# Kernel tuning notes

Measured on AMD Instinct MI355X. Metric: run time of the kernel, lower is better.

Reference implementation:

```python
import jax, jax.numpy as jnp
import numpy as np

EPS = 1e-5
ADJ = 33  # fixed adjusted effective kernel (odd, in [7, 2*ks]); see notes
G, GP = 8, 16  # groups, group_planes


def setup_inputs() -> dict:
    key = jax.random.key(0)
    ks = jax.random.split(key, 6)
    N, C, H, W = 8, 128, 64, 64
    return {
        'x': jax.random.normal(ks[0], (N, C, H, W), jnp.float32),
        'qkv_w': jax.random.normal(ks[1], (2 * C, C), jnp.float32) * (1.0 / np.sqrt(C)),
        'bn_qkv_g': jnp.ones((2 * C,), jnp.float32),
        'bn_qkv_b': jnp.zeros((2 * C,), jnp.float32),
        'base_relative': jax.random.normal(ks[2], (2 * GP, 2 * H - 1, 2 * H - 1), jnp.float32),
        'bn_sim_g': jnp.ones((3 * G,), jnp.float32),
        'bn_sim_b': jnp.zeros((3 * G,), jnp.float32),
        'bn_out_g': jnp.ones((2 * C,), jnp.float32),
        'bn_out_b': jnp.zeros((2 * C,), jnp.float32),
        'in_g': jnp.ones((C,), jnp.float32),
        'in_b': jnp.zeros((C,), jnp.float32),
        'mlp_w1': jax.random.normal(ks[3], (4 * C, C), jnp.float32) * (1.0 / np.sqrt(C)),
        'mlp_w2': jax.random.normal(ks[4], (C, 4 * C), jnp.float32) * (1.0 / np.sqrt(4 * C)),
    }


def _axis_attention(x, qkv_w, bn_qkv_g, bn_qkv_b, base_relative, bn_sim_g, bn_sim_b, bn_out_g, bn_out_b):
    N, C, H, W = x.shape
    out = C
    # height attention: (N,C,H,W) -> (N,W,C,H) -> (N*W, C, H)
    xp = jnp.transpose(x, (0, 3, 1, 2)).reshape(N * W, C, H)
    qkv = jnp.einsum('oc,bcl->bol', qkv_w, xp)
    # BatchNorm1d (training-mode batch stats over (batch, length))
    m = qkv.mean((0, 2), keepdims=True)
    v = qkv.var((0, 2), keepdims=True)
    qkv = (qkv - m) * jax.lax.rsqrt(v + EPS) * bn_qkv_g[None, :, None] + bn_qkv_b[None, :, None]
    qkv = qkv.reshape(N * W, G, 2 * GP, H)
    q, k, vv = qkv[:, :, :GP // 2], qkv[:, :, GP // 2:GP], qkv[:, :, GP:]
    # relative position encodings, bilinear resize (half-pixel == align_corners=False)
    pos = jax.image.resize(base_relative, (2 * GP, ADJ, ADJ), method='bilinear')
    q_e, k_e, v_e = pos[:GP // 2], pos[GP // 2:GP], pos[GP:]
    # resize q/k/v along the attended axis H -> ADJ (1D linear)
    rs = lambda t: jax.image.resize(t, t.shape[:-1] + (ADJ,), method='linear')
    qa, ka, va = rs(q), rs(k), rs(vv)
    qr = jnp.einsum('bgci,cij->bgij', qa, q_e)
    kr = jnp.einsum('bgci,cij->bgij', ka, k_e).transpose(0, 1, 3, 2)
    qk = jnp.einsum('bgci,bgcj->bgij', qa, ka)
    sim = jnp.concatenate([qk, qr, kr], axis=1)  # (N*W, 3G, A, A)
    # BatchNorm2d with per-original-sample stats (torch loop applies BN per b over (W, A, A))
    sim = sim.reshape(N, W, 3 * G, ADJ, ADJ)
    m = sim.mean((1, 3, 4), keepdims=True)
    v2 = sim.var((1, 3, 4), keepdims=True)
    sim = (sim - m) * jax.lax.rsqrt(v2 + EPS) * bn_sim_g[None, None, :, None, None] + bn_sim_b[None, None, :, None, None]
    sim = sim.reshape(N, W, 3, G, ADJ, ADJ).sum(2)  # (N,W,G,A,A)
    # resize similarity maps back to (H,H), then softmax over keys
    sim = jax.image.resize(sim, (N, W, G, H, H), method='bilinear')
    sim = jax.nn.softmax(sim, axis=-1)
    # v embedding resized to (H,H); v resized back to length H
    v_eH = jax.image.resize(v_e, (GP, H, H), method='bilinear')
    vb = jax.image.resize(va, va.shape[:-1] + (H,), method='linear').reshape(N, W, G, GP, H)
    sv = jnp.einsum('nwgij,nwgcj->nwgci', sim, vb)
    sve = jnp.einsum('nwgij,cij->nwgci', sim, v_eH)
    so = jnp.concatenate([sv, sve], axis=-1).reshape(N * W, 2 * out, H)
    m = so.mean((0, 2), keepdims=True)
    v3 = so.var((0, 2), keepdims=True)
    so = (so - m) * jax.lax.rsqrt(v3 + EPS) * bn_out_g[None, :, None] + bn_out_b[None, :, None]
    o = so.reshape(N, W, out, 2, H).sum(3)  # (N,W,out,H)
    return jnp.transpose(o, (0, 2, 3, 1))   # (N,out,H,W)


def _spatial_block(o, in_g, in_b, mlp_w1, mlp_w2):
    N, C, H, W = o.shape
    each = C // 12   # each_direction_channels (deterministic, see notes)
    step = 2         # min(max_dilation=2, min(H,W)//8)
    base = o[:, :each]
    zw = jnp.zeros_like(base[..., :step])
    zh = jnp.zeros_like(base[:, :, :step])
    r = jnp.concatenate([zw, base[..., :-step]], axis=-1)
    l = jnp.concatenate([base[..., step:], zw], axis=-1)
    d = jnp.concatenate([zh, base[:, :, :-step]], axis=2)
    u = jnp.concatenate([base[:, :, step:], zh], axis=2)
    xo = jnp.concatenate([r, l, d, u, o[:, 4 * each:]], axis=1)  # still C channels
    # affine InstanceNorm2d
    m = xo.mean((2, 3), keepdims=True)
    v = xo.var((2, 3), keepdims=True)
    xn = (xo - m) * jax.lax.rsqrt(v + EPS) * in_g[None, :, None, None] + in_b[None, :, None, None]
    h1 = jax.nn.gelu(jnp.einsum('oc,nchw->nohw', mlp_w1, xn), approximate=False)
    return jnp.einsum('oc,nchw->nohw', mlp_w2, h1) + o


def reference(x, qkv_w, bn_qkv_g, bn_qkv_b, base_relative, bn_sim_g, bn_sim_b,
              bn_out_g, bn_out_b, in_g, in_b, mlp_w1, mlp_w2):
    o = _axis_attention(x, qkv_w, bn_qkv_g, bn_qkv_b, base_relative,
                        bn_sim_g, bn_sim_b, bn_out_g, bn_out_b)
    return _spatial_block(o, in_g, in_b, mlp_w1, mlp_w2)
```

## Files before the change

### kernel.cpp

```cpp
#include <hip/hip_runtime.h>
#include <math.h>

constexpr float EPSV = 1e-5f;
typedef unsigned short u16;
using bf16x8 = __attribute__((ext_vector_type(8))) short;
using f32x4  = __attribute__((ext_vector_type(4))) float;

constexpr size_t F_W127  = 0;
constexpr size_t F_W64   = F_W127 + 4224;
constexpr size_t F_QKVST = F_W64  + 2112;
constexpr size_t F_SIMST = F_QKVST+ 512;
constexpr size_t F_SOST  = F_SIMST+ 384;
constexpr size_t F_INST  = F_SOST + 512;
constexpr size_t F_POSTMP= F_INST + 2048;
constexpr size_t F_POS   = F_POSTMP + 134112;
constexpr size_t F_QKV   = F_POS  + 34848;
constexpr size_t F_QKVR  = F_QKV  + 8388608;
constexpr size_t F_SIM   = F_QKVR + 4325376;
constexpr size_t F_PART6 = F_SIM  + 13381632;
constexpr size_t F_VEH   = F_PART6 + 4460544;
constexpr size_t F_XNT   = F_VEH  + 33792;
constexpr size_t F_KET   = F_XNT  + 2097152;
constexpr size_t F_SO    = F_QKV;
constexpr size_t F_XQ    = F_SIM;
constexpr size_t F_BNP2  = F_PART6 + 262144;
constexpr size_t F_WQB   = F_PART6 + 524288;
constexpr size_t F_H1    = F_SIM + 4194304;
constexpr size_t F_W1B   = F_POSTMP;
constexpr size_t F_W2B   = F_POSTMP + 32768;

__device__ __forceinline__ u16 f2b(float x){
  unsigned u = __float_as_uint(x);
  return (u16)((u + 0x7FFFu + ((u>>16)&1u)) >> 16);
}
__device__ __forceinline__ float b2f(u16 v){
  return __uint_as_float((unsigned)v << 16);
}

__device__ __forceinline__ float gelu_f(float v){
  float x = v*0.70710678f;
  float ax = fabsf(x);
  float t = __frcp_rn(1.0f + 0.3275911f*ax);
  float p = 1.061405429f;
  p = p*t - 1.453152027f;
  p = p*t + 1.421413741f;
  p = p*t - 0.284496736f;
  p = p*t + 0.254829592f;
  p = p*t;
  float e = __expf(-ax*ax);
  float y = 1.0f - p*e;
  float er = copysignf(y, x);
  return 0.5f*v*(1.0f + er);
}

struct UpT { int j0[64]; float fj[64]; };
constexpr UpT mkUp(){
  UpT t{};
  for (int o=0;o<64;++o){
    float x = ((float)o + 0.5f)*0.515625f - 0.5f;
    if (x < 0.f) x = 0.f;
    if (x > 32.f) x = 32.f;
    int j = (int)x; if (j > 31) j = 31;
    t.j0[o] = j; t.fj[o] = x - (float)j;
  }
  return t;
}
constexpr UpT UT = mkUp();

__device__ __forceinline__ void upfac(int o, int& j0, float& f){
  float x = ((float)o + 0.5f)*0.515625f - 0.5f;
  x = fminf(fmaxf(x, 0.f), 32.f);
  int j = (int)x; j = j < 31 ? j : 31;
  j0 = j; f = x - (float)j;
}

__device__ __forceinline__ void fma8(float (&a)[8], float qv, const float4& q0, const float4& q1){
  a[0] += qv*q0.x; a[1] += qv*q0.y; a[2] += qv*q0.z; a[3] += qv*q0.w;
  a[4] += qv*q1.x; a[5] += qv*q1.y; a[6] += qv*q1.z; a[7] += qv*q1.w;
}
__device__ __forceinline__ void fma8h(float (&a)[8], float qv, uint4 u){
  a[0] += qv*b2f((u16)(u.x&0xFFFFu)); a[1] += qv*b2f((u16)(u.x>>16));
  a[2] += qv*b2f((u16)(u.y&0xFFFFu)); a[3] += qv*b2f((u16)(u.y>>16));
  a[4] += qv*b2f((u16)(u.z&0xFFFFu)); a[5] += qv*b2f((u16)(u.z>>16));
  a[6] += qv*b2f((u16)(u.w&0xFFFFu)); a[7] += qv*b2f((u16)(u.w>>16));
}

__global__ void k_tables(float* __restrict__ W127, float* __restrict__ W64){
  int i = threadIdx.x;
  if (i < 33){
    const float inv = 127.0f/33.0f;
    float x = ((float)i + 0.5f)*inv - 0.5f;
    float s = 0.f;
    for (int j=0;j<127;++j){ float w = 1.0f - fabsf((float)j - x)/inv; w = fmaxf(w,0.f); W127[i*127+j]=w; s+=w; }
    float r = 1.0f/s;
    for (int j=0;j<127;++j) W127[i*127+j] *= r;
  } else if (i < 66){
    int ii = i-33;
    const float inv = 64.0f/33.0f;
    float x = ((float)ii + 0.5f)*inv - 0.5f;
    float s=0.f;
    for (int j=0;j<64;++j){ float w = 1.0f - fabsf((float)j - x)/inv; w=fmaxf(w,0.f); W64[ii*64+j]=w; s+=w; }
    float r=1.0f/s;
    for (int j=0;j<64;++j) W64[ii*64+j]*=r;
  }
}

__global__ void k_cvtb(const float* __restrict__ src, u16* __restrict__ dst, int n){
  int id = blockIdx.x*256 + threadIdx.x;
  if (id < n) dst[id] = f2b(src[id]);
}

__global__ __launch_bounds__(256) void k_xt(const float* __restrict__ x, u16* __restrict__ xq){
  __shared__ float T[128][66];
  int n = blockIdx.x>>6, h = blockIdx.x&63;
  int tid = threadIdx.x;
  for (int e=tid;e<8192;e+=256){
    int c = e>>6, w = e&63;
    T[c][w] = x[(((size_t)(n*128+c))*64 + h)*64 + w];
  }
  __syncthreads();
  for (int e=tid;e<8192;e+=256){
    int w = e>>7, c = e&127;
    xq[(((size_t)(n*64+w))*64 + h)*128 + c] = f2b(T[c][w]);
  }
}

__global__ __launch_bounds__(256) void k_qkv(const u16* __restrict__ xq, const u16* __restrict__ wqb,
                                             u16* __restrict__ qkvT, float2* __restrict__ part){
  int b = blockIdx.x;
  int tid = threadIdx.x;
  int wv = tid>>6, l = tid&63;
  int wn = wv*64;
  int lr = l&15, lq = l>>4;
  __shared__ u16 As[64*40];
  __shared__ u16 Bs[256*40];
  f32x4 acc[4][4];
  #pragma unroll
  for (int mi=0;mi<4;++mi)
    #pragma unroll
    for (int ni=0;ni<4;++ni) acc[mi][ni] = (f32x4){0.f,0.f,0.f,0.f};
  const u16* Ag = xq + (size_t)b*8192;
  const u16* Bg = wqb;
  for (int ks=0; ks<128; ks+=32){
    __syncthreads();
    { int e = tid; int row = e>>2, q = e&3;
      *(uint4*)&As[row*40 + q*8] = *(const uint4*)&Ag[(size_t)row*128 + ks + q*8]; }
    #pragma unroll
    for (int p=0;p<4;++p){
      int e = tid + p*256; int row = e>>2, q = e&3;
      *(uint4*)&Bs[row*40 + q*8] = *(const uint4*)&Bg[(size_t)row*128 + ks + q*8];
    }
    __syncthreads();
    bf16x8 af[4], bfr[4];
    #pragma unroll
    for (int mi=0;mi<4;++mi) af[mi] = *(const bf16x8*)&As[(mi*16 + lr)*40 + lq*8];
    #pragma unroll
    for (int ni=0;ni<4;++ni) bfr[ni] = *(const bf16x8*)&Bs[(wn + ni*16 + lr)*40 + lq*8];
    #pragma unroll
    for (int mi=0;mi<4;++mi)
      #pragma unroll
      for (int ni=0;ni<4;++ni)
        acc[mi][ni] = __builtin_amdgcn_mfma_f32_16x16x32_bf16(af[mi], bfr[ni], acc[mi][ni], 0,0,0);
  }
  float cs[4] = {0.f,0.f,0.f,0.f}, cq[4] = {0.f,0.f,0.f,0.f};
  u16* ob = qkvT + (size_t)b*16384;
  #pragma unroll
  for (int mi=0;mi<4;++mi)
    #pragma unroll
    for (int r=0;r<4;++r){
      int row = mi*16 + lq*4 + r;
      #pragma unroll
      for (int ni=0;ni<4;++ni){
        float v = acc[mi][ni][r];
        ob[(size_t)row*256 + wn + ni*16 + lr] = f2b(v);
        cs[ni] += v; cq[ni] += v*v;
      }
    }
  #pragma unroll
  for (int ni=0;ni<4;++ni){
    cs[ni] += __shfl_xor(cs[ni], 16); cs[ni] += __shfl_xor(cs[ni], 32);
    cq[ni] += __shfl_xor(cq[ni], 16); cq[ni] += __shfl_xor(cq[ni], 32);
  }
  if (lq == 0){
    #pragma unroll
    for (int ni=0;ni<4;++ni)
      part[(size_t)(wn + ni*16 + lr)*512 + b] = make_float2(cs[ni], cq[ni]);
  }
}

__global__ void k_stats2(const float2* __restrict__ part, const float* __restrict__ g,
                         const float* __restrict__ bta, float2* __restrict__ st){
  int t = threadIdx.x;
  int chL = t>>3, seg = t&7;
  int ch = blockIdx.x*32 + chL;
  float s=0.f, s2=0.f;
  const float2* p = part + (size_t)ch*512 + seg*64;
  #pragma unroll 8
  for (int r=0;r<64;++r){ float2 q = p[r]; s+=q.x; s2+=q.y; }
  __shared__ float A[32][9], Bq[32][9];
  A[chL][seg]=s; Bq[chL][seg]=s2; __syncthreads();
  if (seg==0){
    #pragma unroll
    for (int k=1;k<8;++k){ s += A[chL][k]; s2 += Bq[chL][k]; }
    float m = s*(1.0f/32768.0f);
    float var = s2*(1.0f/32768.0f) - m*m;
    float sc = g[ch]/sqrtf(var + EPSV);
    st[ch] = make_float2(sc, bta[ch] - m*sc);
  }
}

__global__ __launch_bounds__(256) void k_qkvr(const u16* __restrict__ qkvT, const float* __restrict__ W64,
                                              const float2* __restrict__ st, u16* __restrict__ qkvrT){
  int b = blockIdx.x, ch = threadIdx.x;
  const u16* base = qkvT + (size_t)b*16384 + ch;
  float xr[64];
  #pragma unroll
  for (int t=0;t<64;++t) xr[t] = b2f(base[t*256]);
  float2 sb = st[ch];
  u16* ob = qkvrT + (size_t)b*8448 + ch;
  for (int i=0;i<33;++i){
    const float4* wr = (const float4*)(W64 + i*64);
    float a = 0.f;
    #pragma unroll
    for (int q=0;q<16;++q){
      float4 w4 = wr[q];
      a += w4.x*xr[4*q] + w4.y*xr[4*q+1] + w4.z*xr[4*q+2] + w4.w*xr[4*q+3];
    }
    ob[i*256] = f2b(a*sb.x + sb.y);
  }
}

__global__ void k_pos1(const float* __restrict__ base, const float* __restrict__ W127, float* __restrict__ tmp){
  int id = blockIdx.x*256 + threadIdx.x;
  if (id >= 32*33*127) return;
  int c = id / 4191; int r = id - c*4191; int i = r / 127; int xx = r - i*127;
  const float* wr = W127 + i*127;
  const float* bc = base + c*16129 + xx;
  float a=0.f;
  for (int y=0;y<127;++y) a += wr[y]*bc[y*127];
  tmp[id] = a;
}
__global__ void k_pos2(const float* __restrict__ tmp, const float* __restrict__ W127, float* __restrict__ pos){
  int id = blockIdx.x*256 + threadIdx.x;
  if (id >= 32*33*33) return;
  int c = id / 1089; int r = id - c*1089; int i = r / 33; int j = r - i*33;
  const float* wr = W127 + j*127;
  const float* tc = tmp + c*4191 + i*127;
  float a=0.f;
  for (int xx=0;xx<127;++xx) a += wr[xx]*tc[xx];
  pos[id] = a;
}

__global__ void k_keT(const float* __restrict__ pos, float* __restrict__ keT){
  int id = blockIdx.x*256 + threadIdx.x;
  if (id >= 8712) return;
  int c = id / 1089; int r = id - c*1089; int i = r / 33; int j = r - i*33;
  keT[id] = pos[(8+c)*1089 + j*33 + i];
}

__global__ __launch_bounds__(256) void k_sim(const u16* __restrict__ qkvrT, const float* __restrict__ pos,
                                             const float* __restrict__ keT,
                                             u16* __restrict__ sim, float* __restrict__ part6){
  int b = blockIdx.x, g = blockIdx.y;
  __shared__ float lqa[264], lka[264];
  int tid = threadIdx.x;
  for (int e=tid;e<528;e+=256){
    int half = (e < 264) ? 0 : 1;
    int e2 = e - half*264;
    int c = e2/33, i = e2 - c*33;
    float v = b2f(qkvrT[(size_t)b*8448 + i*256 + (g*32 + half*8 + c)]);
    if (half==0) lqa[e2]=v; else lka[e2]=v;
  }
  __syncthreads();
  float sqk=0.f,qqk=0.f,sqr=0.f,qqr=0.f,skr=0.f,qkr=0.f;
  for (int p=tid;p<1089;p+=256){
    int i = p/33, j = p - i*33;
    float qk=0.f, qr=0.f, kr=0.f;
    #pragma unroll
    for (int c=0;c<8;++c){
      float qa_ = lqa[c*33+i];
      float ka_ = lka[c*33+j];
      qk += qa_*ka_;
      qr += qa_*pos[c*1089 + i*33 + j];
      kr += ka_*keT[c*1089 + i*33 + j];
    }
    sim[(size_t)(b*24 + g)*1089 + p] = f2b(qk);
    sim[(size_t)(b*24 + 8 + g)*1089 + p] = f2b(qr);
    sim[(size_t)(b*24 + 16 + g)*1089 + p] = f2b(kr);
    sqk+=qk; qqk+=qk*qk; sqr+=qr; qqr+=qr*qr; skr+=kr; qkr+=kr*kr;
  }
  __shared__ float red[6][256];
  red[0][tid]=sqk; red[1][tid]=qqk; red[2][tid]=sqr;
  red[3][tid]=qqr; red[4][tid]=skr; red[5][tid]=qkr;
  __syncthreads();
  for (int o=128;o>0;o>>=1){
    if (tid<o){
      #pragma unroll
      for (int c=0;c<6;++c) red[c][tid]+=red[c][tid+o];
    }
    __syncthreads();
  }
  if (tid<6) part6[(size_t)(b*8+g)*6 + tid] = red[tid][0];
}

__global__ void k_sstB(const float* __restrict__ part6, const float* __restrict__ g,
                       const float* __restrict__ bta, float2* __restrict__ st){
  int nb = threadIdx.x;
  if (nb >= 192) return;
  int n = nb/24, ch = nb - n*24;
  int t3 = ch>>3, gg = ch&7;
  float s=0.f, s2=0.f;
  for (int w=0; w<64; ++w){
    const float* p = part6 + (size_t)((n*64+w)*8 + gg)*6 + 2*t3;
    s += p[0]; s2 += p[1];
  }
  float m = s*(1.0f/69696.0f);
  float var = s2*(1.0f/69696.0f) - m*m;
  float sc = g[ch]/sqrtf(var + EPSV);
  st[nb] = make_float2(sc, bta[ch] - m*sc);
}

__global__ void k_veP(const float* __restrict__ pos, u16* __restrict__ VeP){
  int id = blockIdx.x*256 + threadIdx.x;
  if (id >= 33792) return;
  int c = id & 15;
  int i = (id >> 4) & 63;
  int k = id >> 10;
  int i0; float fi; upfac(i, i0, fi);
  const float* P = pos + (16+c)*1089;
  VeP[id] = f2b((1.f-fi)*P[i0*33 + k] + fi*P[(i0+1)*33 + k]);
}

__global__ __launch_bounds__(256,4) void k_attn(const u16* __restrict__ sim, const float2* __restrict__ simst,
                                                const u16* __restrict__ qkvrT, const u16* __restrict__ veP,
                                                u16* __restrict__ so){
  int tid = threadIdx.x;
  int wv = tid >> 6;
  int i  = tid & 63;
  int pr   = wv >> 1;
  int half = wv & 1;
  __shared__ float  S[2][1092];
  __shared__ float4 Va[2][132];
  #pragma unroll
  for (int p2=0;p2<2;++p2){
    int bg2 = blockIdx.x*2 + p2;
    int b2 = bg2>>3, g2 = bg2&7, n2 = b2>>6;
    float2 sb0 = simst[n2*24 + g2], sb1 = simst[n2*24 + 8 + g2], sb2 = simst[n2*24 + 16 + g2];
    float badd = sb0.y + sb1.y + sb2.y;
    const u16* s0 = sim + ((size_t)b2*24 + g2)*1089;
    for (int e=tid;e<1089;e+=256)
      S[p2][e] = b2f(s0[e])*sb0.x + b2f(s0[e+8712])*sb1.x + b2f(s0[e+17424])*sb2.x + badd;
    for (int e=tid;e<132;e+=256){
      int j = e>>2, cq = e&3;
      const u16* qp = qkvrT + (size_t)b2*8448 + j*256 + g2*32 + 16 + cq*4;
      uint2 u = *(const uint2*)qp;
      Va[p2][e] = make_float4(b2f((u16)(u.x&0xFFFFu)), b2f((u16)(u.x>>16)),
                              b2f((u16)(u.y&0xFFFFu)), b2f((u16)(u.y>>16)));
    }
  }
  __syncthreads();

  int bg = blockIdx.x*2 + pr;
  int b = bg>>3, g = bg&7;

  int i0; float fi; upfac(i, i0, fi);
  const float* R0 = S[pr] + i0*33;
  float rowv[33];
  #pragma unroll
  for (int k=0;k<33;++k) rowv[k] = R0[k] + fi*(R0[k+33] - R0[k]);
  float qk[33];
  #pragma unroll
  for (int k=0;k<33;++k) qk[k] = 0.f;
  float s = 0.f;
  #pragma unroll
  for (int j=0;j<64;++j){
    float fj = UT.fj[j]; int j0 = UT.j0[j];
    float v = rowv[j0] + fj*(rowv[j0+1] - rowv[j0]);
    float e = __expf(v);
    s += e;
    qk[j0]   += e*(1.f-fj);
    qk[j0+1] += e*fj;
  }
  float inv = 1.f/s;

  float av[8], ae[8];
  #pragma unroll
  for (int c=0;c<8;++c){ av[c]=0.f; ae[c]=0.f; }
  const uint4* vp  = (const uint4*)veP + (size_t)i*2 + half;
  const float4* va4 = &Va[pr][half*2];
  #pragma unroll
  for (int kc=0; kc<33; kc+=11){
    uint4 e0 = vp[(kc+0)*128],  e1 = vp[(kc+1)*128],  e2 = vp[(kc+2)*128];
    uint4 e3 = vp[(kc+3)*128],  e4 = vp[(kc+4)*128],  e5 = vp[(kc+5)*128];
    uint4 e6 = vp[(kc+6)*128],  e7 = vp[(kc+7)*128],  e8 = vp[(kc+8)*128];
    uint4 e9 = vp[(kc+9)*128],  e10= vp[(kc+10)*128];
    #pragma unroll
    for (int t2=0;t2<11;++t2)
      fma8(av, qk[kc+t2], va4[(kc+t2)*4+0], va4[(kc+t2)*4+1]);
    fma8h(ae, qk[kc+0], e0);  fma8h(ae, qk[kc+1], e1);  fma8h(ae, qk[kc+2], e2);
    fma8h(ae, qk[kc+3], e3);  fma8h(ae, qk[kc+4], e4);  fma8h(ae, qk[kc+5], e5);
    fma8h(ae, qk[kc+6], e6);  fma8h(ae, qk[kc+7], e7);  fma8h(ae, qk[kc+8], e8);
    fma8h(ae, qk[kc+9], e9);  fma8h(ae, qk[kc+10], e10);
  }
  u16* ob = so + (size_t)b*16384 + g*2048 + (half*8)*128;
  #pragma unroll
  for (int c=0;c<8;++c){
    ob[c*128 + i]      = f2b(av[c]*inv);
    ob[c*128 + 64 + i] = f2b(ae[c]*inv);
  }
}

__global__ __launch_bounds__(256) void k_sost1(const u16* __restrict__ so, float2* __restrict__ part){
  int ch = blockIdx.x, rowG = blockIdx.y;
  int tid = threadIdx.x;
  int rs = tid>>6, l = tid&63;
  float s=0.f, s2=0.f;
  for (int r = rowG*64 + rs; r < rowG*64 + 64; r += 4){
    float v = b2f(so[((size_t)r*256 + ch)*64 + l]); s+=v; s2+=v*v;
  }
  __shared__ float S1[256], S2[256];
  S1[tid]=s; S2[tid]=s2; __syncthreads();
  for (int o=128;o>0;o>>=1){ if(tid<o){ S1[tid]+=S1[tid+o]; S2[tid]+=S2[tid+o]; } __syncthreads(); }
  if (tid==0) part[ch*8 + rowG] = make_float2(S1[0], S2[0]);
}
__global__ void k_sost2(const float2* __restrict__ part, const float* __restrict__ g,
                        const float* __restrict__ bta, float2* __restrict__ st){
  int ch = threadIdx.x;
  float s=0.f, s2=0.f;
  #pragma unroll
  for (int r=0;r<8;++r){ float2 p = part[ch*8 + r]; s+=p.x; s2+=p.y; }
  float m = s*(1.0f/32768.0f);
  float var = s2*(1.0f/32768.0f) - m*m;
  float sc = g[ch]/sqrtf(var + EPSV);
  st[ch] = make_float2(sc, bta[ch] - m*sc);
}

__global__ __launch_bounds__(256) void k_o(const u16* __restrict__ so, const float2* __restrict__ st,
                                           float* __restrict__ o, float* __restrict__ opart){
  __shared__ float T[64][65];
  __shared__ float R1[256], R2[256];
  int n = blockIdx.x>>7, oc = blockIdx.x&127;
  int tid = threadIdx.x;
  float2 s0 = st[2*oc], s1 = st[2*oc+1];
  float badd = s0.y + s1.y;
  for (int e=tid;e<4096;e+=256){
    int w = e>>6, h = e&63;
    const u16* sb = so + (size_t)(n*64+w)*16384 + (2*oc)*64;
    T[w][h] = b2f(sb[h])*s0.x + b2f(sb[64+h])*s1.x + badd;
  }
  __syncthreads();
  for (int e=tid;e<4096;e+=256){
    int h = e>>6, w = e&63;
    o[(((size_t)(n*128+oc))*64 + h)*64 + w] = T[w][h];
  }
  float fs=0.f, fq=0.f;
  for (int e=tid;e<4096;e+=256){ float v = T[e>>6][e&63]; fs+=v; fq+=v*v; }
  R1[tid]=fs; R2[tid]=fq; __syncthreads();
  for (int o2=128;o2>0;o2>>=1){ if(tid<o2){ R1[tid]+=R1[tid+o2]; R2[tid]+=R2[tid+o2]; } __syncthreads(); }
  float* rec = opart + (size_t)(n*128+oc)*18;
  if (tid==0){ rec[0]=R1[0]; rec[1]=R2[0]; }
  if (tid < 64){
    int l = tid;
    float c0=T[0][l], c1=T[1][l], c62=T[62][l], c63=T[63][l];
    float d0=c0*c0, d1=c1*c1, d62=c62*c62, d63=c63*c63;
    #pragma unroll
    for (int off=32; off; off>>=1){
      c0+=__shfl_xor(c0,off); c1+=__shfl_xor(c1,off);
      c62+=__shfl_xor(c62,off); c63+=__shfl_xor(c63,off);
      d0+=__shfl_xor(d0,off); d1+=__shfl_xor(d1,off);
      d62+=__shfl_xor(d62,off); d63+=__shfl_xor(d63,off);
    }
    if (l==0){
      rec[2]=c0; rec[3]=d0; rec[4]=c1; rec[5]=d1;
      rec[6]=c62; rec[7]=d62; rec[8]=c63; rec[9]=d63;
    }
  } else if (tid < 128){
    int l = tid & 63;
    float r0=T[l][0], r1=T[l][1], r62=T[l][62], r63=T[l][63];
    float e0=r0*r0, e1=r1*r1, e62=r62*r62, e63=r63*r63;
    #pragma unroll
    for (int off=32; off; off>>=1){
      r0+=__shfl_xor(r0,off); r1+=__shfl_xor(r1,off);
      r62+=__shfl_xor(r62,off); r63+=__shfl_xor(r63,off);
      e0+=__shfl_xor(e0,off); e1+=__shfl_xor(e1,off);
      e62+=__shfl_xor(e62,off); e63+=__shfl_xor(e63,off);
    }
    if (l==0){
      rec[10]=r0; rec[11]=e0; rec[12]=r1; rec[13]=e1;
      rec[14]=r62; rec[15]=e62; rec[16]=r63; rec[17]=e63;
    }
  }
}

__global__ void k_instB(const float* __restrict__ opart, const float* __restrict__ g,
                        const float* __restrict__ bta, float2* __restrict__ st){
  int nb = blockIdx.x*256 + threadIdx.x;
  if (nb >= 1024) return;
  int n = nb>>7, c = nb&127;
  float s, q;
  if (c >= 40){
    const float* r = opart + (size_t)(n*128+c)*18;
    s = r[0]; q = r[1];
  } else {
    int grp = c/10, cc = c - grp*10;
    const float* r = opart + (size_t)(n*128+cc)*18;
    if (grp==0){ s = r[0]-r[6]-r[8];   q = r[1]-r[7]-r[9];  }
    else if (grp==1){ s = r[0]-r[2]-r[4];   q = r[1]-r[3]-r[5];  }
    else if (grp==2){ s = r[0]-r[14]-r[16]; q = r[1]-r[15]-r[17];}
    else            { s = r[0]-r[10]-r[12]; q = r[1]-r[11]-r[13];}
  }
  float m = s*(1.0f/4096.0f);
  float var = q*(1.0f/4096.0f) - m*m;
  float sc = g[c]/sqrtf(var + EPSV);
  st[nb] = make_float2(sc, bta[c] - m*sc);
}

__device__ __forceinline__ float xo_val(const float* __restrict__ o, int n, int c, int h, int w){
  if (c >= 40) return o[((n*128 + c)*64 + h)*64 + w];
  int grp = c / 10;
  int cc = c - grp*10;
  int base = (n*128 + cc)*64;
  if (grp==0) return (w>=2) ? o[(base + h)*64 + (w-2)] : 0.f;
  if (grp==1) return (w<62) ? o[(base + h)*64 + (w+2)] : 0.f;
  if (grp==2) return (h>=2) ? o[(base + (h-2))*64 + w] : 0.f;
  return (h<62) ? o[(base + (h+2))*64 + w] : 0.f;
}

__global__ __launch_bounds__(256) void k_xnt(const float* __restrict__ o, const float2* __restrict__ st,
                                             u16* __restrict__ xnT){
  __shared__ float T[64][65];
  int h = blockIdx.x&63, c0 = ((blockIdx.x>>6)&1)*64, n = blockIdx.x>>7;
  int tid = threadIdx.x;
  for (int e=tid;e<4096;e+=256){
    int cL = e>>6, w = e&63;
    float2 sb = st[n*128 + c0+cL];
    T[cL][w] = xo_val(o, n, c0+cL, h, w)*sb.x + sb.y;
  }
  __syncthreads();
  for (int e=tid;e<4096;e+=256){
    int wL = e>>6, cL = e&63;
    xnT[((size_t)(n*4096 + h*64 + wL))*128 + c0 + cL] = f2b(T[cL][wL]);
  }
}

__global__ __launch_bounds__(256) void k_mlp1(const u16* __restrict__ xnT, const u16* __restrict__ w1b,
                                              u16* __restrict__ h1T){
  int hw0 = blockIdx.x*128, co0 = blockIdx.y*64, n = blockIdx.z;
  int tid = threadIdx.x;
  int wv = tid>>6, l = tid&63;
  int wm = (wv>>1)*64, wn = (wv&1)*32;
  int lr = l&15, lq = l>>4;
  __shared__ u16 As[128*40];
  __shared__ u16 Bs[64*40];
  f32x4 acc[4][2];
  #pragma unroll
  for (int mi=0;mi<4;++mi)
    #pragma unroll
    for (int ni=0;ni<2;++ni) acc[mi][ni] = (f32x4){0.f,0.f,0.f,0.f};
  const u16* Ag = xnT + ((size_t)(n*4096 + hw0))*128;
  const u16* Bg = w1b + (size_t)co0*128;
  for (int ks=0; ks<128; ks+=32){
    __syncthreads();
    #pragma unroll
    for (int p=0;p<2;++p){
      int e = tid + p*256; int row = e>>2, q = e&3;
      *(uint4*)&As[row*40 + q*8] = *(const uint4*)&Ag[(size_t)row*128 + ks + q*8];
    }
    { int e = tid; int row = e>>2, q = e&3;
      *(uint4*)&Bs[row*40 + q*8] = *(const uint4*)&Bg[(size_t)row*128 + ks + q*8]; }
    __syncthreads();
    bf16x8 af[4], bfr[2];
    #pragma unroll
    for (int mi=0;mi<4;++mi) af[mi] = *(const bf16x8*)&As[(wm + mi*16 + lr)*40 + lq*8];
    #pragma unroll
    for (int ni=0;ni<2;++ni) bfr[ni] = *(const bf16x8*)&Bs[(wn + ni*16 + lr)*40 + lq*8];
    #pragma unroll
    for (int mi=0;mi<4;++mi)
      #pragma unroll
      for (int ni=0;ni<2;++ni)
        acc[mi][ni] = __builtin_amdgcn_mfma_f32_16x16x32_bf16(af[mi], bfr[ni], acc[mi][ni], 0,0,0);
  }
  u16* ob = h1T + ((size_t)(n*4096 + hw0 + wm))*512 + co0 + wn;
  #pragma unroll
  for (int mi=0;mi<4;++mi)
    #pragma unroll
    for (int r=0;r<4;++r){
      int row = mi*16 + lq*4 + r;
      #pragma unroll
      for (int ni=0;ni<2;++ni){
        float v = acc[mi][ni][r];
        ob[(size_t)row*512 + ni*16 + lr] = f2b(gelu_f(v));
      }
    }
}

__global__ __launch_bounds__(256) void k_mlp2(const u16* __restrict__ w2b, const u16* __restrict__ h1T,
                                              float* __restrict__ out){
  int hw0 = blockIdx.x*64, n = blockIdx.z;
  int ks0 = blockIdx.y*256;
  int tid = threadIdx.x;
  int wv = tid>>6, l = tid&63;
  int wm = (wv>>1)*64, wn = (wv&1)*32;
  int lr = l&15, lq = l>>4;
  __shared__ u16 As[128*40];
  __shared__ u16 Bs[64*40];
  f32x4 acc[4][2];
  #pragma unroll
  for (int mi=0;mi<4;++mi)
    #pragma unroll
    for (int ni=0;ni<2;++ni) acc[mi][ni] = (f32x4){0.f,0.f,0.f,0.f};
  const u16* Ag = w2b;
  const u16* Bg = h1T + ((size_t)(n*4096 + hw0))*512;
  for (int ks=ks0; ks<ks0+256; ks+=32){
    __syncthreads();
    #pragma unroll
    for (int p=0;p<2;++p){
      int e = tid + p*256; int row = e>>2, q = e&3;
      *(uint4*)&As[row*40 + q*8] = *(const uint4*)&Ag[(size_t)row*512 + ks + q*8];
    }
    { int e = tid; int row = e>>2, q = e&3;
      *(uint4*)&Bs[row*40 + q*8] = *(const uint4*)&Bg[(size_t)row*512 + ks + q*8]; }
    __syncthreads();
    bf16x8 af[4], bfr[2];
    #pragma unroll
    for (int mi=0;mi<4;++mi) af[mi] = *(const bf16x8*)&As[(wm + mi*16 + lr)*40 + lq*8];
    #pragma unroll
    for (int ni=0;ni<2;++ni) bfr[ni] = *(const bf16x8*)&Bs[(wn + ni*16 + lr)*40 + lq*8];
    #pragma unroll
    for (int mi=0;mi<4;++mi)
      #pragma unroll
      for (int ni=0;ni<2;++ni)
        acc[mi][ni] = __builtin_amdgcn_mfma_f32_16x16x32_bf16(af[mi], bfr[ni], acc[mi][ni], 0,0,0);
  }
  #pragma unroll
  for (int mi=0;mi<4;++mi)
    #pragma unroll
    for (int r=0;r<4;++r){
      int cout = wm + mi*16 + lq*4 + r;
      #pragma unroll
      for (int ni=0;ni<2;++ni){
        size_t idx = ((size_t)(n*128 + cout))*4096 + hw0 + wn + ni*16 + lr;
        atomicAdd(&out[idx], acc[mi][ni][r]);
      }
    }
}

extern "C" void kernel_launch(void* const* d_in, const int* in_sizes, int n_in,
                              void* d_out, int out_size, void* d_ws, size_t ws_size,
                              hipStream_t stream) {
  (void)in_sizes; (void)n_in; (void)out_size; (void)ws_size;
  const float* x       = (const float*)d_in[0];
  const float* qkvw    = (const float*)d_in[1];
  const float* bng     = (const float*)d_in[2];
  const float* bnb     = (const float*)d_in[3];
  const float* baserel = (const float*)d_in[4];
  const float* simg    = (const float*)d_in[5];
  const float* simb    = (const float*)d_in[6];
  const float* outg    = (const float*)d_in[7];
  const float* outb    = (const float*)d_in[8];
  const float* ing     = (const float*)d_in[9];
  const float* inb     = (const float*)d_in[10];
  const float* w1      = (const float*)d_in[11];
  const float* w2      = (const float*)d_in[12];

  float* ws = (float*)d_ws;
  float*  W127  = ws + F_W127;
  float*  W64   = ws + F_W64;
  float2* qkvst = (float2*)(ws + F_QKVST);
  float2* simst = (float2*)(ws + F_SIMST);
  float2* sost  = (float2*)(ws + F_SOST);
  float2* inst  = (float2*)(ws + F_INST);
  float*  postmp= ws + F_POSTMP;
  float*  pos   = ws + F_POS;
  u16*    qkvT  = (u16*)(ws + F_QKV);
  u16*    qkvrT = (u16*)(ws + F_QKVR);
  u16*    sim   = (u16*)(ws + F_SIM);
  float*  part6 = ws + F_PART6;
  float2* sopart= (float2*)(ws + F_PART6);
  float2* bnp   = (float2*)(ws + F_BNP2);
  float*  opart = ws + F_BNP2;
  u16*    wqb   = (u16*)(ws + F_WQB);
  u16*    veP   = (u16*)(ws + F_VEH);
  u16*    xnT   = (u16*)(ws + F_XNT);
  float*  keT   = ws + F_KET;
  u16*    so    = (u16*)(ws + F_SO);
  u16*    xq    = (u16*)(ws + F_XQ);
  u16*    h1T   = (u16*)(ws + F_H1);
  u16*    w1b   = (u16*)(ws + F_W1B);
  u16*    w2b   = (u16*)(ws + F_W2B);
  float*  out   = (float*)d_out;

  k_tables  <<<dim3(1),        dim3(128), 0, stream>>>(W127, W64);
  k_cvtb    <<<dim3(128),      dim3(256), 0, stream>>>(qkvw, wqb, 32768);
  k_xt      <<<dim3(512),      dim3(256), 0, stream>>>(x, xq);
  k_qkv     <<<dim3(512),      dim3(256), 0, stream>>>(xq, wqb, qkvT, bnp);
  k_stats2  <<<dim3(8),        dim3(256), 0, stream>>>(bnp, bng, bnb, qkvst);
  k_qkvr    <<<dim3(512),      dim3(256), 0, stream>>>(qkvT, W64, qkvst, qkvrT);
  k_pos1    <<<dim3(524),      dim3(256), 0, stream>>>(baserel, W127, postmp);
  k_pos2    <<<dim3(137),      dim3(256), 0, stream>>>(postmp, W127, pos);
  k_keT     <<<dim3(35),       dim3(256), 0, stream>>>(pos, keT);
  k_cvtb    <<<dim3(256),      dim3(256), 0, stream>>>(w1, w1b, 65536);
  k_cvtb    <<<dim3(256),      dim3(256), 0, stream>>>(w2, w2b, 65536);
  k_sim     <<<dim3(512,8),    dim3(256), 0, stream>>>(qkvrT, pos, keT, sim, part6);
  k_sstB    <<<dim3(1),        dim3(192), 0, stream>>>(part6, simg, simb, simst);
  k_veP     <<<dim3(132),      dim3(256), 0, stream>>>(pos, veP);
  k_attn    <<<dim3(2048),     dim3(256), 0, stream>>>(sim, simst, qkvrT, veP, so);
  k_sost1   <<<dim3(256,8),    dim3(256), 0, stream>>>(so, sopart);
  k_sost2   <<<dim3(1),        dim3(256), 0, stream>>>(sopart, outg, outb, sost);
  k_o       <<<dim3(1024),     dim3(256), 0, stream>>>(so, sost, out, opart);
  k_instB   <<<dim3(4),        dim3(256), 0, stream>>>(opart, ing, inb, inst);
  k_xnt     <<<dim3(1024),     dim3(256), 0, stream>>>(out, inst, xnT);
  k_mlp1    <<<dim3(32,8,8),   dim3(256), 0, stream>>>(xnT, w1b, h1T);
  k_mlp2    <<<dim3(64,2,8),   dim3(256), 0, stream>>>(w2b, h1T, out);
}
```

Baseline: 235.9 us.

## Merge independent preprocessing kernels into fewer launches via block-index dispatch

Independent small kernels (table build, weight bf16 conversions, input transpose, QKV GEMM with pos resize pass 1, stats with pos pass 2, qkv resize with keT and VeP) are combined into four launches that branch on block index. The w1b/w2b buffers are moved out of the postmp region because both are now live at the same time. This is meant to cut per-launch overhead and idle tails between tiny dependent launches. In exchange, heterogeneous blocks share one launch configuration, and the larger shared-memory branch may limit occupancy for the simpler branches.

```diff
diff --git a/kernel.cpp b/kernel.cpp
--- a/kernel.cpp
+++ b/kernel.cpp
@@ -26,8 +26,8 @@
 constexpr size_t F_BNP2  = F_PART6 + 262144;
 constexpr size_t F_WQB   = F_PART6 + 524288;
 constexpr size_t F_H1    = F_SIM + 4194304;
-constexpr size_t F_W1B   = F_POSTMP;
-constexpr size_t F_W2B   = F_POSTMP + 32768;
+constexpr size_t F_W1B   = F_PART6 + 1048576;
+constexpr size_t F_W2B   = F_PART6 + 1081344;
 
 __device__ __forceinline__ u16 f2b(float x){
   unsigned u = __float_as_uint(x);
@@ -85,177 +85,203 @@
   a[6] += qv*b2f((u16)(u.w&0xFFFFu)); a[7] += qv*b2f((u16)(u.w>>16));
 }
 
-__global__ void k_tables(float* __restrict__ W127, float* __restrict__ W64){
-  int i = threadIdx.x;
-  if (i < 33){
-    const float inv = 127.0f/33.0f;
-    float x = ((float)i + 0.5f)*inv - 0.5f;
-    float s = 0.f;
-    for (int j=0;j<127;++j){ float w = 1.0f - fabsf((float)j - x)/inv; w = fmaxf(w,0.f); W127[i*127+j]=w; s+=w; }
-    float r = 1.0f/s;
-    for (int j=0;j<127;++j) W127[i*127+j] *= r;
-  } else if (i < 66){
-    int ii = i-33;
-    const float inv = 64.0f/33.0f;
-    float x = ((float)ii + 0.5f)*inv - 0.5f;
-    float s=0.f;
-    for (int j=0;j<64;++j){ float w = 1.0f - fabsf((float)j - x)/inv; w=fmaxf(w,0.f); W64[ii*64+j]=w; s+=w; }
-    float r=1.0f/s;
-    for (int j=0;j<64;++j) W64[ii*64+j]*=r;
-  }
-}
-
-__global__ void k_cvtb(const float* __restrict__ src, u16* __restrict__ dst, int n){
-  int id = blockIdx.x*256 + threadIdx.x;
-  if (id < n) dst[id] = f2b(src[id]);
-}
-
-__global__ __launch_bounds__(256) void k_xt(const float* __restrict__ x, u16* __restrict__ xq){
-  __shared__ float T[128][66];
-  int n = blockIdx.x>>6, h = blockIdx.x&63;
-  int tid = threadIdx.x;
-  for (int e=tid;e<8192;e+=256){
-    int c = e>>6, w = e&63;
-    T[c][w] = x[(((size_t)(n*128+c))*64 + h)*64 + w];
-  }
-  __syncthreads();
-  for (int e=tid;e<8192;e+=256){
-    int w = e>>7, c = e&127;
-    xq[(((size_t)(n*64+w))*64 + h)*128 + c] = f2b(T[c][w]);
-  }
-}
-
-__global__ __launch_bounds__(256) void k_qkv(const u16* __restrict__ xq, const u16* __restrict__ wqb,
-                                             u16* __restrict__ qkvT, float2* __restrict__ part){
-  int b = blockIdx.x;
-  int tid = threadIdx.x;
-  int wv = tid>>6, l = tid&63;
-  int wn = wv*64;
-  int lr = l&15, lq = l>>4;
-  __shared__ u16 As[64*40];
-  __shared__ u16 Bs[256*40];
-  f32x4 acc[4][4];
-  #pragma unroll
-  for (int mi=0;mi<4;++mi)
-    #pragma unroll
-    for (int ni=0;ni<4;++ni) acc[mi][ni] = (f32x4){0.f,0.f,0.f,0.f};
-  const u16* Ag = xq + (size_t)b*8192;
-  const u16* Bg = wqb;
-  for (int ks=0; ks<128; ks+=32){
+__global__ __launch_bounds__(256) void k_pre(const float* __restrict__ x, const float* __restrict__ qkvw,
+                                             const float* __restrict__ w1, const float* __restrict__ w2,
+                                             float* __restrict__ W127, float* __restrict__ W64,
+                                             u16* __restrict__ wqb, u16* __restrict__ w1b,
+                                             u16* __restrict__ w2b, u16* __restrict__ xq){
+  int blk = blockIdx.x, tid = threadIdx.x;
+  if (blk == 0){
+    int i = tid;
+    if (i < 33){
+      const float inv = 127.0f/33.0f;
+      float xx = ((float)i + 0.5f)*inv - 0.5f;
+      float s = 0.f;
+      for (int j=0;j<127;++j){ float w = 1.0f - fabsf((float)j - xx)/inv; w = fmaxf(w,0.f); W127[i*127+j]=w; s+=w; }
+      float r = 1.0f/s;
+      for (int j=0;j<127;++j) W127[i*127+j] *= r;
+    } else if (i < 66){
+      int ii = i-33;
+      const float inv = 64.0f/33.0f;
+      float xx = ((float)ii + 0.5f)*inv - 0.5f;
+      float s=0.f;
+      for (int j=0;j<64;++j){ float w = 1.0f - fabsf((float)j - xx)/inv; w=fmaxf(w,0.f); W64[ii*64+j]=w; s+=w; }
+      float r=1.0f/s;
+      for (int j=0;j<64;++j) W64[ii*64+j]*=r;
+    }
+  } else if (blk < 129){
+    int id = (blk-1)*256 + tid;
+    if (id < 32768) wqb[id] = f2b(qkvw[id]);
+  } else if (blk < 385){
+    int id = (blk-129)*256 + tid;
+    if (id < 65536) w1b[id] = f2b(w1[id]);
+  } else if (blk < 641){
+    int id = (blk-385)*256 + tid;
+    if (id < 65536) w2b[id] = f2b(w2[id]);
+  } else {
+    __shared__ float T[128][66];
+    int bx = blk - 641;
+    int n = bx>>6, h = bx&63;
+    for (int e=tid;e<8192;e+=256){
+      int c = e>>6, w = e&63;
+      T[c][w] = x[(((size_t)(n*128+c))*64 + h)*64 + w];
+    }
     __syncthreads();
-    { int e = tid; int row = e>>2, q = e&3;
-      *(uint4*)&As[row*40 + q*8] = *(const uint4*)&Ag[(size_t)row*128 + ks + q*8]; }
-    #pragma unroll
-    for (int p=0;p<4;++p){
-      int e = tid + p*256; int row = e>>2, q = e&3;
-      *(uint4*)&Bs[row*40 + q*8] = *(const uint4*)&Bg[(size_t)row*128 + ks + q*8];
-    }
-    __syncthreads();
-    bf16x8 af[4], bfr[4];
-    #pragma unroll
-    for (int mi=0;mi<4;++mi) af[mi] = *(const bf16x8*)&As[(mi*16 + lr)*40 + lq*8];
-    #pragma unroll
-    for (int ni=0;ni<4;++ni) bfr[ni] = *(const bf16x8*)&Bs[(wn + ni*16 + lr)*40 + lq*8];
+    for (int e=tid;e<8192;e+=256){
+      int w = e>>7, c = e&127;
+      xq[(((size_t)(n*64+w))*64 + h)*128 + c] = f2b(T[c][w]);
+    }
+  }
+}
+
+__global__ __launch_bounds__(256) void k_qkvp1(const u16* __restrict__ xq, const u16* __restrict__ wqb,
+                                               u16* __restrict__ qkvT, float2* __restrict__ part,
+                                               const float* __restrict__ base, const float* __restrict__ W127,
+                                               float* __restrict__ tmp){
+  if (blockIdx.x < 512){
+    int b = blockIdx.x;
+    int tid = threadIdx.x;
+    int wv = tid>>6, l = tid&63;
+    int wn = wv*64;
+    int lr = l&15, lq = l>>4;
+    __shared__ u16 As[64*40];
+    __shared__ u16 Bs[256*40];
+    f32x4 acc[4][4];
     #pragma unroll
     for (int mi=0;mi<4;++mi)
       #pragma unroll
+      for (int ni=0;ni<4;++ni) acc[mi][ni] = (f32x4){0.f,0.f,0.f,0.f};
+    const u16* Ag = xq + (size_t)b*8192;
+    const u16* Bg = wqb;
+    for (int ks=0; ks<128; ks+=32){
+      __syncthreads();
+      { int e = tid; int row = e>>2, q = e&3;
+        *(uint4*)&As[row*40 + q*8] = *(const uint4*)&Ag[(size_t)row*128 + ks + q*8]; }
+      #pragma unroll
+      for (int p=0;p<4;++p){
+        int e = tid + p*256; int row = e>>2, q = e&3;
+        *(uint4*)&Bs[row*40 + q*8] = *(const uint4*)&Bg[(size_t)row*128 + ks + q*8];
+      }
+      __syncthreads();
+      bf16x8 af[4], bfr[4];
+      #pragma unroll
+      for (int mi=0;mi<4;++mi) af[mi] = *(const bf16x8*)&As[(mi*16 + lr)*40 + lq*8];
+      #pragma unroll
+      for (int ni=0;ni<4;++ni) bfr[ni] = *(const bf16x8*)&Bs[(wn + ni*16 + lr)*40 + lq*8];
+      #pragma unroll
+      for (int mi=0;mi<4;++mi)
+        #pragma unroll
+        for (int ni=0;ni<4;++ni)
+          acc[mi][ni] = __builtin_amdgcn_mfma_f32_16x16x32_bf16(af[mi], bfr[ni], acc[mi][ni], 0,0,0);
+    }
+    float cs[4] = {0.f,0.f,0.f,0.f}, cq[4] = {0.f,0.f,0.f,0.f};
+    u16* ob = qkvT + (size_t)b*16384;
+    #pragma unroll
+    for (int mi=0;mi<4;++mi)
+      #pragma unroll
+      for (int r=0;r<4;++r){
+        int row = mi*16 + lq*4 + r;
+        #pragma unroll
+        for (int ni=0;ni<4;++ni){
+          float v = acc[mi][ni][r];
+          ob[(size_t)row*256 + wn + ni*16 + lr] = f2b(v);
+          cs[ni] += v; cq[ni] += v*v;
+        }
+      }
+    #pragma unroll
+    for (int ni=0;ni<4;++ni){
+      cs[ni] += __shfl_xor(cs[ni], 16); cs[ni] += __shfl_xor(cs[ni], 32);
+      cq[ni] += __shfl_xor(cq[ni], 16); cq[ni] += __shfl_xor(cq[ni], 32);
+    }
+    if (lq == 0){
+      #pragma unroll
       for (int ni=0;ni<4;++ni)
-        acc[mi][ni] = __builtin_amdgcn_mfma_f32_16x16x32_bf16(af[mi], bfr[ni], acc[mi][ni], 0,0,0);
-  }
-  float cs[4] = {0.f,0.f,0.f,0.f}, cq[4] = {0.f,0.f,0.f,0.f};
-  u16* ob = qkvT + (size_t)b*16384;
-  #pragma unroll
-  for (int mi=0;mi<4;++mi)
-    #pragma unroll
-    for (int r=0;r<4;++r){
-      int row = mi*16 + lq*4 + r;
-      #pragma unroll
-      for (int ni=0;ni<4;++ni){
-        float v = acc[mi][ni][r];
-        ob[(size_t)row*256 + wn + ni*16 + lr] = f2b(v);
-        cs[ni] += v; cq[ni] += v*v;
+        part[(size_t)(wn + ni*16 + lr)*512 + b] = make_float2(cs[ni], cq[ni]);
+    }
+  } else {
+    int id = (blockIdx.x-512)*256 + threadIdx.x;
+    if (id >= 32*33*127) return;
+    int c = id / 4191; int r = id - c*4191; int i = r / 127; int xx = r - i*127;
+    const float* wr = W127 + i*127;
+    const float* bc = base + c*16129 + xx;
+    float a=0.f;
+    for (int y=0;y<127;++y) a += wr[y]*bc[y*127];
+    tmp[id] = a;
+  }
+}
+
+__global__ __launch_bounds__(256) void k_st2p2(const float2* __restrict__ part, const float* __restrict__ g,
+                                               const float* __restrict__ bta, float2* __restrict__ st,
+                                               const float* __restrict__ tmp, const float* __restrict__ W127,
+                                               float* __restrict__ pos){
+  if (blockIdx.x < 8){
+    int t = threadIdx.x;
+    int chL = t>>3, seg = t&7;
+    int ch = blockIdx.x*32 + chL;
+    float s=0.f, s2=0.f;
+    const float2* p = part + (size_t)ch*512 + seg*64;
+    #pragma unroll 8
+    for (int r=0;r<64;++r){ float2 q = p[r]; s+=q.x; s2+=q.y; }
+    __shared__ float A[32][9], Bq[32][9];
+    A[chL][seg]=s; Bq[chL][seg]=s2; __syncthreads();
+    if (seg==0){
+      #pragma unroll
+      for (int k=1;k<8;++k){ s += A[chL][k]; s2 += Bq[chL][k]; }
+      float m = s*(1.0f/32768.0f);
+      float var = s2*(1.0f/32768.0f) - m*m;
+      float sc = g[ch]/sqrtf(var + EPSV);
+      st[ch] = make_float2(sc, bta[ch] - m*sc);
+    }
+  } else {
+    int id = (blockIdx.x-8)*256 + threadIdx.x;
+    if (id >= 32*33*33) return;
+    int c = id / 1089; int r = id - c*1089; int i = r / 33; int j = r - i*33;
+    const float* wr = W127 + j*127;
+    const float* tc = tmp + c*4191 + i*127;
+    float a=0.f;
+    for (int xx=0;xx<127;++xx) a += wr[xx]*tc[xx];
+    pos[id] = a;
+  }
+}
+
+__global__ __launch_bounds__(256) void k_qkvr_kv(const u16* __restrict__ qkvT, const float* __restrict__ W64,
+                                                 const float2* __restrict__ st, u16* __restrict__ qkvrT,
+                                                 const float* __restrict__ pos, float* __restrict__ keT,
+                                                 u16* __restrict__ VeP){
+  int blk = blockIdx.x;
+  if (blk < 512){
+    int b = blk, ch = threadIdx.x;
+    const u16* base = qkvT + (size_t)b*16384 + ch;
+    float xr[64];
+    #pragma unroll
+    for (int t=0;t<64;++t) xr[t] = b2f(base[t*256]);
+    float2 sb = st[ch];
+    u16* ob = qkvrT + (size_t)b*8448 + ch;
+    for (int i=0;i<33;++i){
+      const float4* wr = (const float4*)(W64 + i*64);
+      float a = 0.f;
+      #pragma unroll
+      for (int q=0;q<16;++q){
+        float4 w4 = wr[q];
+        a += w4.x*xr[4*q] + w4.y*xr[4*q+1] + w4.z*xr[4*q+2] + w4.w*xr[4*q+3];
       }
-    }
-  #pragma unroll
-  for (int ni=0;ni<4;++ni){
-    cs[ni] += __shfl_xor(cs[ni], 16); cs[ni] += __shfl_xor(cs[ni], 32);
-    cq[ni] += __shfl_xor(cq[ni], 16); cq[ni] += __shfl_xor(cq[ni], 32);
-  }
-  if (lq == 0){
-    #pragma unroll
-    for (int ni=0;ni<4;++ni)
-      part[(size_t)(wn + ni*16 + lr)*512 + b] = make_float2(cs[ni], cq[ni]);
-  }
-}
-
-__global__ void k_stats2(const float2* __restrict__ part, const float* __restrict__ g,
-                         const float* __restrict__ bta, float2* __restrict__ st){
-  int t = threadIdx.x;
-  int chL = t>>3, seg = t&7;
-  int ch = blockIdx.x*32 + chL;
-  float s=0.f, s2=0.f;
-  const float2* p = part + (size_t)ch*512 + seg*64;
-  #pragma unroll 8
-  for (int r=0;r<64;++r){ float2 q = p[r]; s+=q.x; s2+=q.y; }
-  __shared__ float A[32][9], Bq[32][9];
-  A[chL][seg]=s; Bq[chL][seg]=s2; __syncthreads();
-  if (seg==0){
-    #pragma unroll
-    for (int k=1;k<8;++k){ s += A[chL][k]; s2 += Bq[chL][k]; }
-    float m = s*(1.0f/32768.0f);
-    float var = s2*(1.0f/32768.0f) - m*m;
-    float sc = g[ch]/sqrtf(var + EPSV);
-    st[ch] = make_float2(sc, bta[ch] - m*sc);
-  }
-}
-
-__global__ __launch_bounds__(256) void k_qkvr(const u16* __restrict__ qkvT, const float* __restrict__ W64,
-                                              const float2* __restrict__ st, u16* __restrict__ qkvrT){
-  int b = blockIdx.x, ch = threadIdx.x;
-  const u16* base = qkvT + (size_t)b*16384 + ch;
-  float xr[64];
-  #pragma unroll
-  for (int t=0;t<64;++t) xr[t] = b2f(base[t*256]);
-  float2 sb = st[ch];
-  u16* ob = qkvrT + (size_t)b*8448 + ch;
-  for (int i=0;i<33;++i){
-    const float4* wr = (const float4*)(W64 + i*64);
-    float a = 0.f;
-    #pragma unroll
-    for (int q=0;q<16;++q){
-      float4 w4 = wr[q];
-      a += w4.x*xr[4*q] + w4.y*xr[4*q+1] + w4.z*xr[4*q+2] + w4.w*xr[4*q+3];
-    }
-    ob[i*256] = f2b(a*sb.x + sb.y);
-  }
-}
-
-__global__ void k_pos1(const float* __restrict__ base, const float* __restrict__ W127, float* __restrict__ tmp){
-  int id = blockIdx.x*256 + threadIdx.x;
-  if (id >= 32*33*127) return;
-  int c = id / 4191; int r = id - c*4191; int i = r / 127; int xx = r - i*127;
-  const float* wr = W127 + i*127;
-  const float* bc = base + c*16129 + xx;
-  float a=0.f;
-  for (int y=0;y<127;++y) a += wr[y]*bc[y*127];
-  tmp[id] = a;
-}
-__global__ void k_pos2(const float* __restrict__ tmp, const float* __restrict__ W127, float* __restrict__ pos){
-  int id = blockIdx.x*256 + threadIdx.x;
-  if (id >= 32*33*33) return;
-  int c = id / 1089; int r = id - c*1089; int i = r / 33; int j = r - i*33;
-  const float* wr = W127 + j*127;
-  const float* tc = tmp + c*4191 + i*127;
-  float a=0.f;
-  for (int xx=0;xx<127;++xx) a += wr[xx]*tc[xx];
-  pos[id] = a;
-}
-
-__global__ void k_keT(const float* __restrict__ pos, float* __restrict__ keT){
-  int id = blockIdx.x*256 + threadIdx.x;
-  if (id >= 8712) return;
-  int c = id / 1089; int r = id - c*1089; int i = r / 33; int j = r - i*33;
-  keT[id] = pos[(8+c)*1089 + j*33 + i];
+      ob[i*256] = f2b(a*sb.x + sb.y);
+    }
+  } else if (blk < 547){
+    int id = (blk-512)*256 + threadIdx.x;
+    if (id >= 8712) return;
+    int c = id / 1089; int r = id - c*1089; int i = r / 33; int j = r - i*33;
+    keT[id] = pos[(8+c)*1089 + j*33 + i];
+  } else {
+    int id = (blk-547)*256 + threadIdx.x;
+    if (id >= 33792) return;
+    int c = id & 15;
+    int i = (id >> 4) & 63;
+    int k = id >> 10;
+    int i0; float fi; upfac(i, i0, fi);
+    const float* P = pos + (16+c)*1089;
+    VeP[id] = f2b((1.f-fi)*P[i0*33 + k] + fi*P[(i0+1)*33 + k]);
+  }
 }
 
 __global__ __launch_bounds__(256) void k_sim(const u16* __restrict__ qkvrT, const float* __restrict__ pos,
@@ -318,17 +344,6 @@
   float var = s2*(1.0f/69696.0f) - m*m;
   float sc = g[ch]/sqrtf(var + EPSV);
   st[nb] = make_float2(sc, bta[ch] - m*sc);
-}
-
-__global__ void k_veP(const float* __restrict__ pos, u16* __restrict__ VeP){
-  int id = blockIdx.x*256 + threadIdx.x;
-  if (id >= 33792) return;
-  int c = id & 15;
-  int i = (id >> 4) & 63;
-  int k = id >> 10;
-  int i0; float fi; upfac(i, i0, fi);
-  const float* P = pos + (16+c)*1089;
-  VeP[id] = f2b((1.f-fi)*P[i0*33 + k] + fi*P[(i0+1)*33 + k]);
 }
 
 __global__ __launch_bounds__(256,4) void k_attn(const u16* __restrict__ sim, const float2* __restrict__ simst,
@@ -690,20 +705,12 @@
   u16*    w2b   = (u16*)(ws + F_W2B);
   float*  out   = (float*)d_out;
 
-  k_tables  <<<dim3(1),        dim3(128), 0, stream>>>(W127, W64);
-  k_cvtb    <<<dim3(128),      dim3(256), 0, stream>>>(qkvw, wqb, 32768);
-  k_xt      <<<dim3(512),      dim3(256), 0, stream>>>(x, xq);
-  k_qkv     <<<dim3(512),      dim3(256), 0, stream>>>(xq, wqb, qkvT, bnp);
-  k_stats2  <<<dim3(8),        dim3(256), 0, stream>>>(bnp, bng, bnb, qkvst);
-  k_qkvr    <<<dim3(512),      dim3(256), 0, stream>>>(qkvT, W64, qkvst, qkvrT);
-  k_pos1    <<<dim3(524),      dim3(256), 0, stream>>>(baserel, W127, postmp);
-  k_pos2    <<<dim3(137),      dim3(256), 0, stream>>>(postmp, W127, pos);
-  k_keT     <<<dim3(35),       dim3(256), 0, stream>>>(pos, keT);
-  k_cvtb    <<<dim3(256),      dim3(256), 0, stream>>>(w1, w1b, 65536);
-  k_cvtb    <<<dim3(256),      dim3(256), 0, stream>>>(w2, w2b, 65536);
+  k_pre     <<<dim3(1153),     dim3(256), 0, stream>>>(x, qkvw, w1, w2, W127, W64, wqb, w1b, w2b, xq);
+  k_qkvp1   <<<dim3(1036),     dim3(256), 0, stream>>>(xq, wqb, qkvT, bnp, baserel, W127, postmp);
+  k_st2p2   <<<dim3(145),      dim3(256), 0, stream>>>(bnp, bng, bnb, qkvst, postmp, W127, pos);
+  k_qkvr_kv <<<dim3(679),      dim3(256), 0, stream>>>(qkvT, W64, qkvst, qkvrT, pos, keT, veP);
   k_sim     <<<dim3(512,8),    dim3(256), 0, stream>>>(qkvrT, pos, keT, sim, part6);
   k_sstB    <<<dim3(1),        dim3(192), 0, stream>>>(part6, simg, simb, simst);
-  k_veP     <<<dim3(132),      dim3(256), 0, stream>>>(pos, veP);
   k_attn    <<<dim3(2048),     dim3(256), 0, stream>>>(sim, simst, qkvrT, veP, so);
   k_sost1   <<<dim3(256,8),    dim3(256), 0, stream>>>(so, sopart);
   k_sost2   <<<dim3(1),        dim3(256), 0, stream>>>(sopart, outg, outb, sost);
```

New measurement: 210.9 us, median of 2. 1.12x faster.
